# Optimization experiments

Measured on AMD Instinct MI355X. Metric: run time of the kernel, lower is better.

The kernel has to match this reference:

```python
import jax, jax.numpy as jnp
import numpy as np
from jax import lax

B, CIN, H, W = 16, 128, 56, 56
COUT, K, STRIDE, PAD, DIL = 256, 3, 1, 1, 1
D = 8  # lattice.d
KE = K * K
M = CIN * KE // D  # sub-vectors per spatial position


def setup_inputs() -> dict:
    key = jax.random.key(0)
    k1, k2, k3 = jax.random.split(key, 3)
    input_encodings = jax.random.normal(k1, (B, CIN, H, W), dtype=jnp.float32)
    weight_encodings = jax.random.normal(k2, (COUT, M, D), dtype=jnp.float32)
    bias = jax.random.normal(k3, (COUT,), dtype=jnp.float32)
    return {"input_encodings": input_encodings,
            "weight_encodings": weight_encodings,
            "bias": bias}


def reference(input_encodings, weight_encodings, bias):
    b, cin, h, w = input_encodings.shape
    cout, m, d = weight_encodings.shape
    h_out = (h + 2 * PAD - DIL * (K - 1) - 1) // STRIDE + 1
    w_out = (w + 2 * PAD - DIL * (K - 1) - 1) // STRIDE + 1
    L = h_out * w_out
    # im2col / unfold: (B, Cin*K*K, Hout, Wout), channel-major (c, kh, kw) ordering
    patches = lax.conv_general_dilated_patches(
        input_encodings, (K, K), (STRIDE, STRIDE), [(PAD, PAD), (PAD, PAD)],
        rhs_dilation=(DIL, DIL))
    # (B, L, M, D): each position split into M lattice-encoded sub-vectors of dim D
    x = patches.reshape(b, cin * K * K, L).transpose(0, 2, 1).reshape(b, L, m, d)
    # two-sided vLUT matrix multiply == sum of per-sub-vector inner products
    out = jnp.einsum('blmd,omd->bol', x, weight_encodings)  # (B, Cout, L)
    out = out.reshape(b, cout, h_out, w_out)
    return out + bias[None, :, None, None]
```

## Files before the change

kernel.cpp:

```cpp
#include <hip/hip_runtime.h>
#include <hip/hip_bf16.h>

#define CIN_   128
#define HW_    56
#define LHW_   3136
#define COUT_  256
#define KTOT_  1152

typedef unsigned short u16;
typedef __attribute__((ext_vector_type(8))) short short8v;
typedef __attribute__((ext_vector_type(4))) float f32x4;

__device__ __forceinline__ u16 f2bf(float f) {
  union { float f; unsigned u; } v; v.f = f;
  unsigned u = v.u;
  u += 0x7fffu + ((u >> 16) & 1u);
  return (u16)(u >> 16);
}
__device__ __forceinline__ unsigned pack2(u16 a, u16 b) {
  return (unsigned)a | ((unsigned)b << 16);
}

__global__ void wreorder2_kernel(const float* __restrict__ w, u16* __restrict__ wb,
                                 u16* __restrict__ zp) {
  if (blockIdx.x == 0 && threadIdx.x < 16) {
    uint4 z; z.x = z.y = z.z = z.w = 0u;
    reinterpret_cast<uint4*>(zp)[threadIdx.x] = z;
  }
  int j = blockIdx.x * 256 + threadIdx.x;
  int c4 = j & 31;
  int o  = (j >> 5) & 255;
  int t  = j >> 13;
  int c0i = c4 >> 3;
  int lg  = (c4 >> 1) & 3;
  size_t slot = ((size_t)(t * 4 + c0i) * 16 + (o >> 4)) * 64 + lg * 16 + (o & 15);
  const float* src = w + (size_t)o * KTOT_ + t;
  ushort4 r;
  r.x = f2bf(src[(c4 * 4 + 0) * 9]);
  r.y = f2bf(src[(c4 * 4 + 1) * 9]);
  r.z = f2bf(src[(c4 * 4 + 2) * 9]);
  r.w = f2bf(src[(c4 * 4 + 3) * 9]);
  *reinterpret_cast<ushort4*>(wb + slot * 8 + (c4 & 1) * 4) = r;
}

__global__ void wreorder_kernel(const float* __restrict__ w, u16* __restrict__ wb) {
  int j = blockIdx.x * 256 + threadIdx.x;
  int c4 = j & 31;
  int o  = (j >> 5) & 255;
  int t  = j >> 13;
  const float* src = w + (size_t)o * KTOT_ + t;
  ushort4 r;
  r.x = f2bf(src[(c4 * 4 + 0) * 9]);
  r.y = f2bf(src[(c4 * 4 + 1) * 9]);
  r.z = f2bf(src[(c4 * 4 + 2) * 9]);
  r.w = f2bf(src[(c4 * 4 + 3) * 9]);
  *reinterpret_cast<ushort4*>(wb + ((size_t)(t * 256 + o) * 128 + c4 * 4)) = r;
}

#define TLDSW_ 136
__global__ __launch_bounds__(256) void nhwc_kernel(
    const float* __restrict__ in, u16* __restrict__ xin) {
  __shared__ u16 ts[64 * TLDSW_];
  const int bp = blockIdx.x;
  const int b = bp / 49;
  const int pos0 = (bp % 49) * 64;
  const int tid = threadIdx.x;
  const float* ib = in + (size_t)b * CIN_ * LHW_ + pos0;
  {
    const int p  = tid & 63;
    const int c0 = (tid >> 6) * 32;
    #pragma unroll
    for (int i = 0; i < 32; ++i)
      ts[p * TLDSW_ + c0 + i] = f2bf(ib[(size_t)(c0 + i) * LHW_ + p]);
  }
  __syncthreads();
  {
    const int p  = tid >> 2;
    const int c0 = (tid & 3) * 32;
    u16* dst = xin + ((size_t)b * LHW_ + pos0 + p) * CIN_ + c0;
    const u16* srcr = &ts[p * TLDSW_ + c0];
    #pragma unroll
    for (int j = 0; j < 4; ++j)
      reinterpret_cast<uint4*>(dst)[j] =
          *reinterpret_cast<const uint4*>(srcr + j * 8);
  }
}

__device__ __forceinline__ void gload_lds16(const void* g, void* l) {
  __builtin_amdgcn_global_load_lds(
      (const __attribute__((address_space(1))) void*)g,
      (__attribute__((address_space(3))) void*)l, 16, 0, 0);
}

__global__ __launch_bounds__(256, 3) void conv6_kernel(
    const u16* __restrict__ xin, const u16* __restrict__ wb2,
    const float* __restrict__ bias, const u16* __restrict__ zpage,
    float* __restrict__ out)
{
  __shared__ __align__(16) u16 alds[2][4096];
  __shared__ __align__(16) u16 blds[2][4096];

  const int tid  = threadIdx.x;
  const int lane = tid & 63;
  const int wid  = tid >> 6;
  const int wc   = wid & 1;
  const int ws   = wid >> 1;
  const int lr   = lane & 15;
  const int lg   = lane >> 4;

  const int g   = (blockIdx.x & 7) * 98 + (blockIdx.x >> 3);
  const int coh = g & 1;
  const int nt  = g >> 1;

  const int p   = tid & 127;
  const int lgi = tid >> 7;
  const int n   = nt * 128 + p;
  const int bb  = n / LHW_;
  const int ll  = n - bb * LHW_;
  const int py  = ll / HW_;
  const int px  = ll - py * HW_;
  const u16* bsrc0 = xin + (size_t)n * CIN_ + lgi * 8;

  auto stage = [&](int ks, int h) {
    {
      const u16* s0 = wb2 + ((size_t)ks * 1024 + coh * 512 + tid) * 8;
      gload_lds16(s0,        &alds[h][(size_t)(tid & ~63) * 8]);
      gload_lds16(s0 + 2048, &alds[h][(size_t)((tid + 256) & ~63) * 8]);
    }
    {
      const int t   = ks >> 2;
      const int c0i = ks & 3;
      const int dy  = t / 3;
      const int dx  = t - dy * 3;
      const int yy  = py + dy - 1;
      const int xx  = px + dx - 1;
      const bool ok = ((unsigned)yy < (unsigned)HW_) & ((unsigned)xx < (unsigned)HW_);
      const u16* sB  = ok ? bsrc0 + ((dy - 1) * HW_ + (dx - 1)) * CIN_ + c0i * 32
                          : zpage;
      const u16* sB1 = ok ? sB + 16 : zpage;
      gload_lds16(sB,  &blds[h][(size_t)(tid & ~63) * 8]);
      gload_lds16(sB1, &blds[h][(size_t)((tid + 256) & ~63) * 8]);
    }
  };

  f32x4 acc[4][4];
  #pragma unroll
  for (int i = 0; i < 4; ++i)
    #pragma unroll
    for (int j = 0; j < 4; ++j)
      acc[i][j] = f32x4{0.f, 0.f, 0.f, 0.f};

  stage(0, 0);
  __syncthreads();

  #pragma unroll 1
  for (int ks = 0; ks < 36; ++ks) {
    const int h = ks & 1;
    if (ks < 35) stage(ks + 1, h ^ 1);

    short8v a[4], b[4];
    #pragma unroll
    for (int ai = 0; ai < 4; ++ai)
      a[ai] = *reinterpret_cast<const short8v*>(
          &alds[h][(size_t)((wc * 4 + ai) * 64 + lg * 16 + lr) * 8]);
    #pragma unroll
    for (int nj = 0; nj < 4; ++nj)
      b[nj] = *reinterpret_cast<const short8v*>(
          &blds[h][(size_t)(lg * 128 + ws * 64 + nj * 16 + lr) * 8]);

    #pragma unroll
    for (int ai = 0; ai < 4; ++ai)
      #pragma unroll
      for (int nj = 0; nj < 4; ++nj)
        acc[ai][nj] = __builtin_amdgcn_mfma_f32_16x16x32_bf16(
            a[ai], b[nj], acc[ai][nj], 0, 0, 0);

    __syncthreads();
  }

  #pragma unroll
  for (int nj = 0; nj < 4; ++nj) {
    const int nb0 = nt * 128 + ws * 64 + nj * 16;
    const int ob  = nb0 / LHW_;
    const int ol  = nb0 - ob * LHW_;
    float* obp = out + (size_t)ob * COUT_ * LHW_ + ol + lr;
    #pragma unroll
    for (int ai = 0; ai < 4; ++ai) {
      #pragma unroll
      for (int rr = 0; rr < 4; ++rr) {
        const int o = coh * 128 + wc * 64 + ai * 16 + lg * 4 + rr;
        obp[(size_t)o * LHW_] = acc[ai][nj][rr] + bias[o];
      }
    }
  }
}

#define NF_    7
#define SCOLS_ 58
#define SPP_   232
#define CSTR_  128
__global__ __launch_bounds__(256, 2) void conv2_kernel(
    const float* __restrict__ in, const u16* __restrict__ wb,
    const float* __restrict__ bias, float* __restrict__ out)
{
  __shared__ u16 xs[SPP_ * CSTR_];
  const int tid  = threadIdx.x;
  const int lane = tid & 63;
  const int wid  = tid >> 6;
  const int lr   = lane & 15;
  const int lg   = lane >> 4;
  const int bid = blockIdx.x;
  const int ch  = bid & 1;
  const int ty  = (bid >> 1) % 28;
  const int b   = bid / 56;
  const float* inb = in + (size_t)b * CIN_ * LHW_;
  const int iy0 = ty * 2 - 1;

  #pragma unroll 1
  for (int i = 0; i < 15; ++i) {
    int idx = i * 256 + tid;
    if (idx < SPP_ * 16) {
      int cg  = idx / SPP_;
      int spp = idx - cg * SPP_;
      int rr  = spp / SCOLS_;
      int cc  = spp - rr * SCOLS_;
      int iy  = iy0 + rr;
      int ix  = cc - 1;
      bool ok = ((unsigned)iy < (unsigned)HW_) && ((unsigned)ix < (unsigned)HW_);
      const float* pp = inb + (size_t)cg * 8 * LHW_ + iy * HW_ + ix;
      u16 v[8];
      #pragma unroll
      for (int jj = 0; jj < 8; ++jj)
        v[jj] = f2bf(ok ? pp[jj * LHW_] : 0.f);
      uint4 pk;
      pk.x = pack2(v[0], v[1]); pk.y = pack2(v[2], v[3]);
      pk.z = pack2(v[4], v[5]); pk.w = pack2(v[6], v[7]);
      *reinterpret_cast<uint4*>(&xs[spp * CSTR_ + ((cg * 8) ^ ((spp & 7) << 3))]) = pk;
    }
  }
  int spp0[NF_];
  #pragma unroll
  for (int nf = 0; nf < NF_; ++nf) {
    int sp = nf * 16 + lr;
    int r  = (sp >= 56) ? 1 : 0;
    int x  = sp - r * 56;
    spp0[nf] = (r + 1) * SCOLS_ + x + 1;
  }
  f32x4 acc[2][NF_];
  #pragma unroll
  for (int m = 0; m < 2; ++m)
    #pragma unroll
    for (int nf = 0; nf < NF_; ++nf)
      acc[m][nf] = f32x4{0.f, 0.f, 0.f, 0.f};
  __syncthreads();
  const u16* wt0 = wb + (size_t)(ch * 128 + wid * 32 + lr) * CSTR_ + lg * 8;
  #pragma unroll 1
  for (int t = 0; t < 9; ++t) {
    const int dspp = (t / 3 - 1) * SCOLS_ + (t % 3 - 1);
    const u16* wt = wt0 + (size_t)t * 256 * CSTR_;
    #pragma unroll
    for (int c0i = 0; c0i < 4; ++c0i) {
      const int c0 = c0i * 32;
      short8v a0 = *reinterpret_cast<const short8v*>(wt + c0);
      short8v a1 = *reinterpret_cast<const short8v*>(wt + 16 * CSTR_ + c0);
      short8v bv[NF_];
      #pragma unroll
      for (int nf = 0; nf < NF_; ++nf) {
        int spp = spp0[nf] + dspp;
        int off = spp * CSTR_ + ((c0 + lg * 8) ^ ((spp & 7) << 3));
        bv[nf] = *reinterpret_cast<const short8v*>(&xs[off]);
      }
      #pragma unroll
      for (int nf = 0; nf < NF_; ++nf) {
        acc[0][nf] = __builtin_amdgcn_mfma_f32_16x16x32_bf16(a0, bv[nf], acc[0][nf], 0, 0, 0);
        acc[1][nf] = __builtin_amdgcn_mfma_f32_16x16x32_bf16(a1, bv[nf], acc[1][nf], 0, 0, 0);
      }
    }
  }
  float* ob = out + (size_t)b * COUT_ * LHW_ + ty * 112;
  const int obase = ch * 128 + wid * 32 + lg * 4;
  #pragma unroll
  for (int m = 0; m < 2; ++m)
    #pragma unroll
    for (int rr = 0; rr < 4; ++rr) {
      const int o = obase + m * 16 + rr;
      const float bs = bias[o];
      #pragma unroll
      for (int nf = 0; nf < NF_; ++nf)
        ob[(size_t)o * LHW_ + nf * 16 + lr] = acc[m][nf][rr] + bs;
    }
}

#define SPT0_  64
#define BK0_   32
#define NKS0_  36
#define LDSW0_ 40
__global__ __launch_bounds__(256, 2) void conv_fb_kernel(
    const float* __restrict__ in, const float* __restrict__ wf,
    const float* __restrict__ bias, float* __restrict__ out)
{
  __shared__ u16 xs[SPT0_ * LDSW0_];
  const int tid = threadIdx.x;
  const int lane = tid & 63;
  const int wid = tid >> 6;
  const int lg = lane >> 4;
  const int lr = lane & 15;
  const int bid = blockIdx.x;
  const int b = bid / 49;
  const int l0 = (bid % 49) * SPT0_;
  const int sp = tid & 63;
  const int qq = tid >> 6;
  const int l = l0 + sp;
  const int y = l / HW_;
  const int x = l - y * HW_;
  const float* inb = in + (size_t)b * CIN_ * LHW_;
  f32x4 acc[4][4];
  #pragma unroll
  for (int i = 0; i < 4; ++i)
    #pragma unroll
    for (int j = 0; j < 4; ++j) acc[i][j] = f32x4{0.f, 0.f, 0.f, 0.f};
  auto stage_load = [&](int ks) -> uint4 {
    int kbase = ks * BK0_ + qq * 8;
    int c = kbase / 9;
    int t = kbase - c * 9;
    u16 v[8];
    #pragma unroll
    for (int j = 0; j < 8; ++j) {
      int dy = (t * 11) >> 5;
      int dx = t - 3 * dy;
      int yy = y + dy - 1, xx = x + dx - 1;
      float f = 0.f;
      if ((unsigned)yy < (unsigned)HW_ && (unsigned)xx < (unsigned)HW_)
        f = inb[(c * HW_ + yy) * HW_ + xx];
      v[j] = f2bf(f);
      ++t; if (t == 9) { t = 0; ++c; }
    }
    uint4 r;
    r.x = pack2(v[0], v[1]); r.y = pack2(v[2], v[3]);
    r.z = pack2(v[4], v[5]); r.w = pack2(v[6], v[7]);
    return r;
  };
  uint4 st = stage_load(0);
  for (int ks = 0; ks < NKS0_; ++ks) {
    __syncthreads();
    *reinterpret_cast<uint4*>(&xs[sp * LDSW0_ + qq * 8]) = st;
    __syncthreads();
    if (ks + 1 < NKS0_) st = stage_load(ks + 1);
    const int k0 = ks * BK0_;
    short8v a[4];
    #pragma unroll
    for (int ai = 0; ai < 4; ++ai) {
      const int o = wid * 64 + ai * 16 + lr;
      const float* pp = wf + (size_t)o * KTOT_ + k0 + lg * 8;
      u16 t8[8];
      #pragma unroll
      for (int j = 0; j < 8; ++j) t8[j] = f2bf(pp[j]);
      union { uint4 u; short8v s; } cv;
      cv.u.x = pack2(t8[0], t8[1]); cv.u.y = pack2(t8[2], t8[3]);
      cv.u.z = pack2(t8[4], t8[5]); cv.u.w = pack2(t8[6], t8[7]);
      a[ai] = cv.s;
    }
    short8v bv[4];
    #pragma unroll
    for (int sj = 0; sj < 4; ++sj)
      bv[sj] = *reinterpret_cast<const short8v*>(&xs[(sj * 16 + lr) * LDSW0_ + lg * 8]);
    #pragma unroll
    for (int ai = 0; ai < 4; ++ai)
      #pragma unroll
      for (int sj = 0; sj < 4; ++sj)
        acc[ai][sj] = __builtin_amdgcn_mfma_f32_16x16x32_bf16(a[ai], bv[sj], acc[ai][sj], 0, 0, 0);
  }
  float* outb = out + (size_t)b * COUT_ * LHW_ + l0;
  #pragma unroll
  for (int ai = 0; ai < 4; ++ai)
    #pragma unroll
    for (int r = 0; r < 4; ++r) {
      const int o = wid * 64 + ai * 16 + lg * 4 + r;
      const float bvs = bias[o];
      #pragma unroll
      for (int sj = 0; sj < 4; ++sj)
        outb[(size_t)o * LHW_ + sj * 16 + lr] = acc[ai][sj][r] + bvs;
    }
}

extern "C" void kernel_launch(void* const* d_in, const int* in_sizes, int n_in,
                              void* d_out, int out_size, void* d_ws, size_t ws_size,
                              hipStream_t stream) {
  (void)in_sizes; (void)n_in; (void)out_size;
  const float* in   = (const float*)d_in[0];
  const float* w    = (const float*)d_in[1];
  const float* bias = (const float*)d_in[2];
  float* out = (float*)d_out;

  const size_t wbytes  = (size_t)COUT_ * KTOT_ * sizeof(u16);
  const size_t xbytes  = (size_t)16 * LHW_ * CIN_ * sizeof(u16);
  const size_t need    = wbytes + xbytes + 256;

  if (ws_size >= need) {
    u16* wb2 = (u16*)d_ws;
    u16* xin = wb2 + wbytes / 2;
    u16* zp  = xin + xbytes / 2;
    wreorder2_kernel<<<dim3(288), dim3(256), 0, stream>>>(w, wb2, zp);
    nhwc_kernel<<<dim3(784), dim3(256), 0, stream>>>(in, xin);
    conv6_kernel<<<dim3(784), dim3(256), 0, stream>>>(xin, wb2, bias, zp, out);
  } else if (ws_size >= wbytes) {
    u16* wb = (u16*)d_ws;
    wreorder_kernel<<<dim3(288), dim3(256), 0, stream>>>(w, wb);
    conv2_kernel<<<dim3(896), dim3(256), 0, stream>>>(in, wb, bias, out);
  } else {
    conv_fb_kernel<<<dim3(784), dim3(256), 0, stream>>>(in, w, bias, out);
  }
}
```

Baseline: 70.03 us.

## Enlarge conv tile to 256x256 with 8-wave blocks and phased MFMA schedule

Replaces the 128x128-tile implicit-GEMM conv kernel with a 512-thread, 256(cout)x256(positions) tile that covers all output channels per block and uses a K-step of 64. Weights are re-laid out to match, and each k-step is split into four MFMA phases separated by barriers, with ds_reads interleaved and s_setprio raised around the MFMAs. The aim is more data reuse per LDS load, fewer k-iterations and better MFMA/memory overlap. In exchange it uses a 128 KB LDS double buffer and 32 accumulator tiles per wave, and launches only 196 blocks, which is below one block per CU on a 256-CU part.

After: 79.31 us. 1.13x slower.

```diff
diff --git a/kernel.cpp b/kernel.cpp
--- a/kernel.cpp
+++ b/kernel.cpp
@@ -21,26 +21,26 @@
   return (unsigned)a | ((unsigned)b << 16);
 }
 
-__global__ void wreorder2_kernel(const float* __restrict__ w, u16* __restrict__ wb,
+__global__ void wreorder3_kernel(const float* __restrict__ w, u16* __restrict__ wb3,
                                  u16* __restrict__ zp) {
   if (blockIdx.x == 0 && threadIdx.x < 16) {
     uint4 z; z.x = z.y = z.z = z.w = 0u;
     reinterpret_cast<uint4*>(zp)[threadIdx.x] = z;
   }
   int j = blockIdx.x * 256 + threadIdx.x;
-  int c4 = j & 31;
-  int o  = (j >> 5) & 255;
-  int t  = j >> 13;
-  int c0i = c4 >> 3;
-  int lg  = (c4 >> 1) & 3;
-  size_t slot = ((size_t)(t * 4 + c0i) * 16 + (o >> 4)) * 64 + lg * 16 + (o & 15);
-  const float* src = w + (size_t)o * KTOT_ + t;
+  int half = j & 1;
+  int s    = j >> 1;
+  int o    = s & 255;
+  int kg8  = s >> 8;
+  int kt   = kg8 >> 3;
+  int kgrp = kg8 & 7;
+  int t    = kt >> 1;
+  int c    = ((kt & 1) << 6) + kgrp * 8 + half * 4;
+  const float* src = w + (size_t)o * KTOT_ + (size_t)c * 9 + t;
   ushort4 r;
-  r.x = f2bf(src[(c4 * 4 + 0) * 9]);
-  r.y = f2bf(src[(c4 * 4 + 1) * 9]);
-  r.z = f2bf(src[(c4 * 4 + 2) * 9]);
-  r.w = f2bf(src[(c4 * 4 + 3) * 9]);
-  *reinterpret_cast<ushort4*>(wb + slot * 8 + (c4 & 1) * 4) = r;
+  r.x = f2bf(src[0]);  r.y = f2bf(src[9]);
+  r.z = f2bf(src[18]); r.w = f2bf(src[27]);
+  *reinterpret_cast<ushort4*>(wb3 + (size_t)s * 8 + half * 4) = r;
 }
 
 __global__ void wreorder_kernel(const float* __restrict__ w, u16* __restrict__ wb) {
@@ -92,107 +92,140 @@
       (__attribute__((address_space(3))) void*)l, 16, 0, 0);
 }
 
-__global__ __launch_bounds__(256, 3) void conv6_kernel(
-    const u16* __restrict__ xin, const u16* __restrict__ wb2,
+__global__ __launch_bounds__(512, 2) void conv7_kernel(
+    const u16* __restrict__ xin, const u16* __restrict__ wb3,
     const float* __restrict__ bias, const u16* __restrict__ zpage,
     float* __restrict__ out)
 {
-  __shared__ __align__(16) u16 alds[2][4096];
-  __shared__ __align__(16) u16 blds[2][4096];
+  __shared__ __align__(16) u16 alds[2][16384];
+  __shared__ __align__(16) u16 blds[2][16384];
 
   const int tid  = threadIdx.x;
   const int lane = tid & 63;
   const int wid  = tid >> 6;
-  const int wc   = wid & 1;
-  const int ws   = wid >> 1;
+  const int wm   = wid & 1;
+  const int wn   = wid >> 1;
   const int lr   = lane & 15;
   const int lg   = lane >> 4;
 
-  const int g   = (blockIdx.x & 7) * 98 + (blockIdx.x >> 3);
-  const int coh = g & 1;
-  const int nt  = g >> 1;
-
-  const int p   = tid & 127;
-  const int lgi = tid >> 7;
-  const int n   = nt * 128 + p;
-  const int bb  = n / LHW_;
-  const int ll  = n - bb * LHW_;
+  const int nt = blockIdx.x;
+
+  const int sp  = tid & 255;
+  const int kg0 = tid >> 8;
+  const int n   = nt * 256 + sp;
+  const int ll  = n % LHW_;
   const int py  = ll / HW_;
   const int px  = ll - py * HW_;
-  const u16* bsrc0 = xin + (size_t)n * CIN_ + lgi * 8;
-
-  auto stage = [&](int ks, int h) {
-    {
-      const u16* s0 = wb2 + ((size_t)ks * 1024 + coh * 512 + tid) * 8;
-      gload_lds16(s0,        &alds[h][(size_t)(tid & ~63) * 8]);
-      gload_lds16(s0 + 2048, &alds[h][(size_t)((tid + 256) & ~63) * 8]);
-    }
-    {
-      const int t   = ks >> 2;
-      const int c0i = ks & 3;
-      const int dy  = t / 3;
-      const int dx  = t - dy * 3;
-      const int yy  = py + dy - 1;
-      const int xx  = px + dx - 1;
-      const bool ok = ((unsigned)yy < (unsigned)HW_) & ((unsigned)xx < (unsigned)HW_);
-      const u16* sB  = ok ? bsrc0 + ((dy - 1) * HW_ + (dx - 1)) * CIN_ + c0i * 32
-                          : zpage;
-      const u16* sB1 = ok ? sB + 16 : zpage;
-      gload_lds16(sB,  &blds[h][(size_t)(tid & ~63) * 8]);
-      gload_lds16(sB1, &blds[h][(size_t)((tid + 256) & ~63) * 8]);
-    }
+  const u16* xpos = xin + (size_t)n * CIN_ + (kg0 << 3);
+  unsigned okm = 0;
+  #pragma unroll
+  for (int t = 0; t < 9; ++t) {
+    int yy = py + t / 3 - 1, xx = px + t % 3 - 1;
+    if ((unsigned)yy < (unsigned)HW_ && (unsigned)xx < (unsigned)HW_)
+      okm |= 1u << t;
+  }
+
+  const int ldsoff = (tid & ~63) * 8;
+
+  auto stage = [&](int kt, int h) {
+    const u16* sa = wb3 + ((size_t)kt * 2048 + tid) * 8;
+    u16* da = alds[h] + ldsoff;
+    #pragma unroll
+    for (int q = 0; q < 4; ++q)
+      gload_lds16(sa + q * 4096, da + q * 4096);
+    const int t    = kt >> 1;
+    const int dy   = t / 3, dx = t - dy * 3;
+    const int doff = ((dy - 1) * HW_ + (dx - 1)) * CIN_ + ((kt & 1) << 6);
+    const bool ok  = (okm >> t) & 1;
+    const u16* sb  = ok ? xpos + doff : zpage;
+    u16* db = blds[h] + ldsoff;
+    #pragma unroll
+    for (int q = 0; q < 4; ++q)
+      gload_lds16(sb + q * 16, db + q * 4096);
   };
 
-  f32x4 acc[4][4];
-  #pragma unroll
-  for (int i = 0; i < 4; ++i)
+  const int abase = (lg * 256 + wm * 128 + lr) * 8;
+  const int bbase = (lg * 256 + wn * 64 + lr) * 8;
+
+  f32x4 acc[8][4];
+  #pragma unroll
+  for (int i = 0; i < 8; ++i)
     #pragma unroll
     for (int j = 0; j < 4; ++j)
       acc[i][j] = f32x4{0.f, 0.f, 0.f, 0.f};
 
+  short8v Af[8];
+  short8v Bf0[4], Bf1[4];
+
+#define READ_A(h, half)                                                         \
+  { _Pragma("unroll") for (int kk = 0; kk < 2; ++kk)                            \
+    _Pragma("unroll") for (int ai = 0; ai < 4; ++ai)                            \
+      Af[kk * 4 + ai] = *reinterpret_cast<const short8v*>(                      \
+          &alds[h][abase + kk * 8192 + ((half) * 4 + ai) * 128]); }
+#define READ_B(h, half, Bf)                                                     \
+  { _Pragma("unroll") for (int kk = 0; kk < 2; ++kk)                            \
+    _Pragma("unroll") for (int nj = 0; nj < 2; ++nj)                            \
+      (Bf)[kk * 2 + nj] = *reinterpret_cast<const short8v*>(                    \
+          &blds[h][bbase + kk * 8192 + ((half) * 2 + nj) * 128]); }
+#define PHASE_SYNC()                                                            \
+  __builtin_amdgcn_sched_barrier(0);                                            \
+  __builtin_amdgcn_s_barrier();                                                 \
+  asm volatile("s_waitcnt lgkmcnt(0)" ::: "memory");                            \
+  __builtin_amdgcn_sched_barrier(0);
+#define MFMA16(ah, bh, Bf)                                                      \
+  { __builtin_amdgcn_s_setprio(1);                                              \
+    _Pragma("unroll") for (int kk = 0; kk < 2; ++kk)                            \
+    _Pragma("unroll") for (int ai = 0; ai < 4; ++ai)                            \
+    _Pragma("unroll") for (int nj = 0; nj < 2; ++nj)                            \
+      acc[(ah) * 4 + ai][(bh) * 2 + nj] = __builtin_amdgcn_mfma_f32_16x16x32_bf16( \
+          Af[kk * 4 + ai], (Bf)[kk * 2 + nj], acc[(ah) * 4 + ai][(bh) * 2 + nj], \
+          0, 0, 0);                                                             \
+    __builtin_amdgcn_s_setprio(0);                                              \
+    __builtin_amdgcn_sched_barrier(0);                                          \
+    __builtin_amdgcn_s_barrier(); }
+
   stage(0, 0);
-  __syncthreads();
+  asm volatile("s_waitcnt vmcnt(0)" ::: "memory");
+  __builtin_amdgcn_s_barrier();
 
   #pragma unroll 1
-  for (int ks = 0; ks < 36; ++ks) {
-    const int h = ks & 1;
-    if (ks < 35) stage(ks + 1, h ^ 1);
-
-    short8v a[4], b[4];
-    #pragma unroll
-    for (int ai = 0; ai < 4; ++ai)
-      a[ai] = *reinterpret_cast<const short8v*>(
-          &alds[h][(size_t)((wc * 4 + ai) * 64 + lg * 16 + lr) * 8]);
-    #pragma unroll
-    for (int nj = 0; nj < 4; ++nj)
-      b[nj] = *reinterpret_cast<const short8v*>(
-          &blds[h][(size_t)(lg * 128 + ws * 64 + nj * 16 + lr) * 8]);
-
-    #pragma unroll
-    for (int ai = 0; ai < 4; ++ai)
-      #pragma unroll
-      for (int nj = 0; nj < 4; ++nj)
-        acc[ai][nj] = __builtin_amdgcn_mfma_f32_16x16x32_bf16(
-            a[ai], b[nj], acc[ai][nj], 0, 0, 0);
-
-    __syncthreads();
+  for (int kt = 0; kt < 18; ++kt) {
+    const int h = kt & 1;
+    if (kt < 17) stage(kt + 1, h ^ 1);
+    READ_A(h, 0); READ_B(h, 0, Bf0);
+    PHASE_SYNC();
+    MFMA16(0, 0, Bf0);
+    READ_B(h, 1, Bf1);
+    PHASE_SYNC();
+    MFMA16(0, 1, Bf1);
+    READ_A(h, 1);
+    PHASE_SYNC();
+    MFMA16(1, 0, Bf0);
+    MFMA16(1, 1, Bf1);
+    asm volatile("s_waitcnt vmcnt(0)" ::: "memory");
+    __builtin_amdgcn_s_barrier();
   }
 
   #pragma unroll
   for (int nj = 0; nj < 4; ++nj) {
-    const int nb0 = nt * 128 + ws * 64 + nj * 16;
+    const int nb0 = nt * 256 + wn * 64 + nj * 16;
     const int ob  = nb0 / LHW_;
     const int ol  = nb0 - ob * LHW_;
     float* obp = out + (size_t)ob * COUT_ * LHW_ + ol + lr;
     #pragma unroll
-    for (int ai = 0; ai < 4; ++ai) {
-      #pragma unroll
-      for (int rr = 0; rr < 4; ++rr) {
-        const int o = coh * 128 + wc * 64 + ai * 16 + lg * 4 + rr;
-        obp[(size_t)o * LHW_] = acc[ai][nj][rr] + bias[o];
-      }
-    }
-  }
+    for (int ai = 0; ai < 8; ++ai) {
+      const int o = wm * 128 + ai * 16 + lg * 4;
+      const float4 bs = *reinterpret_cast<const float4*>(&bias[o]);
+      obp[(size_t)(o + 0) * LHW_] = acc[ai][nj][0] + bs.x;
+      obp[(size_t)(o + 1) * LHW_] = acc[ai][nj][1] + bs.y;
+      obp[(size_t)(o + 2) * LHW_] = acc[ai][nj][2] + bs.z;
+      obp[(size_t)(o + 3) * LHW_] = acc[ai][nj][3] + bs.w;
+    }
+  }
+#undef READ_A
+#undef READ_B
+#undef PHASE_SYNC
+#undef MFMA16
 }
 
 #define NF_    7
@@ -397,12 +430,12 @@
   const size_t need    = wbytes + xbytes + 256;
 
   if (ws_size >= need) {
-    u16* wb2 = (u16*)d_ws;
-    u16* xin = wb2 + wbytes / 2;
+    u16* wb3 = (u16*)d_ws;
+    u16* xin = wb3 + wbytes / 2;
     u16* zp  = xin + xbytes / 2;
-    wreorder2_kernel<<<dim3(288), dim3(256), 0, stream>>>(w, wb2, zp);
+    wreorder3_kernel<<<dim3(288), dim3(256), 0, stream>>>(w, wb3, zp);
     nhwc_kernel<<<dim3(784), dim3(256), 0, stream>>>(in, xin);
-    conv6_kernel<<<dim3(784), dim3(256), 0, stream>>>(xin, wb2, bias, zp, out);
+    conv7_kernel<<<dim3(196), dim3(512), 0, stream>>>(xin, wb3, bias, zp, out);
   } else if (ws_size >= wbytes) {
     u16* wb = (u16*)d_ws;
     wreorder_kernel<<<dim3(288), dim3(256), 0, stream>>>(w, wb);
```

## Restructure conv weight layout, merge barriers, precompute halo mask in implicit GEMM

Applied to the files above, without the earlier changes.

Reorders the packed bf16 weights into a new layout so the A and B LDS tiles share the same per-thread staging offset and fragment addressing. The main loop now waits on vmcnt and hits one barrier per k-step before issuing the next stage, instead of two __syncthreads. The 3x3 boundary-validity mask is precomputed once per thread, and bias is loaded as float4. Occupancy is raised to 4 blocks per SM. Having only one barrier depends on correct double-buffer ordering, and the higher launch bound may squeeze registers.

Measured after the change: 69.98 us. Within noise of the previous version (-0.1%).

```diff
diff --git a/kernel.cpp b/kernel.cpp
--- a/kernel.cpp
+++ b/kernel.cpp
@@ -21,26 +21,25 @@
   return (unsigned)a | ((unsigned)b << 16);
 }
 
-__global__ void wreorder2_kernel(const float* __restrict__ w, u16* __restrict__ wb,
+__global__ void wreorder5_kernel(const float* __restrict__ w, u16* __restrict__ wb5,
                                  u16* __restrict__ zp) {
   if (blockIdx.x == 0 && threadIdx.x < 16) {
     uint4 z; z.x = z.y = z.z = z.w = 0u;
     reinterpret_cast<uint4*>(zp)[threadIdx.x] = z;
   }
   int j = blockIdx.x * 256 + threadIdx.x;
-  int c4 = j & 31;
-  int o  = (j >> 5) & 255;
-  int t  = j >> 13;
-  int c0i = c4 >> 3;
-  int lg  = (c4 >> 1) & 3;
-  size_t slot = ((size_t)(t * 4 + c0i) * 16 + (o >> 4)) * 64 + lg * 16 + (o & 15);
-  const float* src = w + (size_t)o * KTOT_ + t;
+  int half = j & 1;
+  int s    = j >> 1;
+  int o    = s & 255;
+  int kgrp = (s >> 8) & 3;
+  int kt   = s >> 10;
+  int t    = kt >> 2;
+  int ch   = (kt & 3) * 32 + kgrp * 8 + half * 4;
+  const float* src = w + (size_t)o * KTOT_ + (size_t)ch * 9 + t;
   ushort4 r;
-  r.x = f2bf(src[(c4 * 4 + 0) * 9]);
-  r.y = f2bf(src[(c4 * 4 + 1) * 9]);
-  r.z = f2bf(src[(c4 * 4 + 2) * 9]);
-  r.w = f2bf(src[(c4 * 4 + 3) * 9]);
-  *reinterpret_cast<ushort4*>(wb + slot * 8 + (c4 & 1) * 4) = r;
+  r.x = f2bf(src[0]);  r.y = f2bf(src[9]);
+  r.z = f2bf(src[18]); r.w = f2bf(src[27]);
+  *reinterpret_cast<ushort4*>(wb5 + (size_t)s * 8 + half * 4) = r;
 }
 
 __global__ void wreorder_kernel(const float* __restrict__ w, u16* __restrict__ wb) {
@@ -92,8 +91,8 @@
       (__attribute__((address_space(3))) void*)l, 16, 0, 0);
 }
 
-__global__ __launch_bounds__(256, 3) void conv6_kernel(
-    const u16* __restrict__ xin, const u16* __restrict__ wb2,
+__global__ __launch_bounds__(256, 4) void conv12_kernel(
+    const u16* __restrict__ xin, const u16* __restrict__ wb5,
     const float* __restrict__ bias, const u16* __restrict__ zpage,
     float* __restrict__ out)
 {
@@ -103,8 +102,8 @@
   const int tid  = threadIdx.x;
   const int lane = tid & 63;
   const int wid  = tid >> 6;
-  const int wc   = wid & 1;
-  const int ws   = wid >> 1;
+  const int wm   = wid & 1;
+  const int wn   = wid >> 1;
   const int lr   = lane & 15;
   const int lg   = lane >> 4;
 
@@ -113,35 +112,38 @@
   const int nt  = g >> 1;
 
   const int p   = tid & 127;
-  const int lgi = tid >> 7;
+  const int kga = tid >> 7;
   const int n   = nt * 128 + p;
-  const int bb  = n / LHW_;
-  const int ll  = n - bb * LHW_;
+  const int ll  = n % LHW_;
   const int py  = ll / HW_;
   const int px  = ll - py * HW_;
-  const u16* bsrc0 = xin + (size_t)n * CIN_ + lgi * 8;
-
-  auto stage = [&](int ks, int h) {
-    {
-      const u16* s0 = wb2 + ((size_t)ks * 1024 + coh * 512 + tid) * 8;
-      gload_lds16(s0,        &alds[h][(size_t)(tid & ~63) * 8]);
-      gload_lds16(s0 + 2048, &alds[h][(size_t)((tid + 256) & ~63) * 8]);
-    }
-    {
-      const int t   = ks >> 2;
-      const int c0i = ks & 3;
-      const int dy  = t / 3;
-      const int dx  = t - dy * 3;
-      const int yy  = py + dy - 1;
-      const int xx  = px + dx - 1;
-      const bool ok = ((unsigned)yy < (unsigned)HW_) & ((unsigned)xx < (unsigned)HW_);
-      const u16* sB  = ok ? bsrc0 + ((dy - 1) * HW_ + (dx - 1)) * CIN_ + c0i * 32
-                          : zpage;
-      const u16* sB1 = ok ? sB + 16 : zpage;
-      gload_lds16(sB,  &blds[h][(size_t)(tid & ~63) * 8]);
-      gload_lds16(sB1, &blds[h][(size_t)((tid + 256) & ~63) * 8]);
-    }
+  const u16* xp = xin + (size_t)n * CIN_ + kga * 8;
+  unsigned okm = 0;
+  #pragma unroll
+  for (int t = 0; t < 9; ++t) {
+    int yy = py + t / 3 - 1, xx = px + t % 3 - 1;
+    if ((unsigned)yy < (unsigned)HW_ && (unsigned)xx < (unsigned)HW_)
+      okm |= 1u << t;
+  }
+
+  const int ldso = (tid & ~63) * 8;
+
+  auto stage = [&](int kt, int h) {
+    const u16* sa = wb5 + ((size_t)kt * 1024 + kga * 256 + coh * 128 + p) * 8;
+    gload_lds16(sa,        alds[h] + ldso);
+    gload_lds16(sa + 4096, alds[h] + ldso + 2048);
+    const int t    = kt >> 2;
+    const int dy   = t / 3, dx = t - dy * 3;
+    const int doff = ((dy - 1) * HW_ + (dx - 1)) * CIN_ + ((kt & 3) << 5);
+    const bool ok  = (okm >> t) & 1;
+    const u16* sb  = ok ? xp + doff : zpage;
+    const u16* sb1 = ok ? sb + 16 : zpage;
+    gload_lds16(sb,  blds[h] + ldso);
+    gload_lds16(sb1, blds[h] + ldso + 2048);
   };
+
+  const int abase = (lg * 128 + wm * 64 + lr) * 8;
+  const int bbase = (lg * 128 + wn * 64 + lr) * 8;
 
   f32x4 acc[4][4];
   #pragma unroll
@@ -151,46 +153,45 @@
       acc[i][j] = f32x4{0.f, 0.f, 0.f, 0.f};
 
   stage(0, 0);
-  __syncthreads();
 
   #pragma unroll 1
-  for (int ks = 0; ks < 36; ++ks) {
-    const int h = ks & 1;
-    if (ks < 35) stage(ks + 1, h ^ 1);
-
-    short8v a[4], b[4];
+  for (int kt = 0; kt < 36; ++kt) {
+    const int h = kt & 1;
+    asm volatile("s_waitcnt vmcnt(0)" ::: "memory");
+    __builtin_amdgcn_s_barrier();
+    asm volatile("" ::: "memory");
+    if (kt < 35) stage(kt + 1, h ^ 1);
+
+    short8v a[4], bv[4];
     #pragma unroll
     for (int ai = 0; ai < 4; ++ai)
-      a[ai] = *reinterpret_cast<const short8v*>(
-          &alds[h][(size_t)((wc * 4 + ai) * 64 + lg * 16 + lr) * 8]);
+      a[ai] = *reinterpret_cast<const short8v*>(&alds[h][abase + ai * 128]);
     #pragma unroll
     for (int nj = 0; nj < 4; ++nj)
-      b[nj] = *reinterpret_cast<const short8v*>(
-          &blds[h][(size_t)(lg * 128 + ws * 64 + nj * 16 + lr) * 8]);
-
+      bv[nj] = *reinterpret_cast<const short8v*>(&blds[h][bbase + nj * 128]);
     #pragma unroll
     for (int ai = 0; ai < 4; ++ai)
       #pragma unroll
       for (int nj = 0; nj < 4; ++nj)
         acc[ai][nj] = __builtin_amdgcn_mfma_f32_16x16x32_bf16(
-            a[ai], b[nj], acc[ai][nj], 0, 0, 0);
-
-    __syncthreads();
+            a[ai], bv[nj], acc[ai][nj], 0, 0, 0);
+    asm volatile("" ::: "memory");
   }
 
   #pragma unroll
   for (int nj = 0; nj < 4; ++nj) {
-    const int nb0 = nt * 128 + ws * 64 + nj * 16;
+    const int nb0 = nt * 128 + wn * 64 + nj * 16;
     const int ob  = nb0 / LHW_;
     const int ol  = nb0 - ob * LHW_;
     float* obp = out + (size_t)ob * COUT_ * LHW_ + ol + lr;
     #pragma unroll
     for (int ai = 0; ai < 4; ++ai) {
-      #pragma unroll
-      for (int rr = 0; rr < 4; ++rr) {
-        const int o = coh * 128 + wc * 64 + ai * 16 + lg * 4 + rr;
-        obp[(size_t)o * LHW_] = acc[ai][nj][rr] + bias[o];
-      }
+      const int o = coh * 128 + wm * 64 + ai * 16 + lg * 4;
+      const float4 bs = *reinterpret_cast<const float4*>(&bias[o]);
+      obp[(size_t)(o + 0) * LHW_] = acc[ai][nj][0] + bs.x;
+      obp[(size_t)(o + 1) * LHW_] = acc[ai][nj][1] + bs.y;
+      obp[(size_t)(o + 2) * LHW_] = acc[ai][nj][2] + bs.z;
+      obp[(size_t)(o + 3) * LHW_] = acc[ai][nj][3] + bs.w;
     }
   }
 }
@@ -397,12 +398,12 @@
   const size_t need    = wbytes + xbytes + 256;
 
   if (ws_size >= need) {
-    u16* wb2 = (u16*)d_ws;
-    u16* xin = wb2 + wbytes / 2;
+    u16* wb5 = (u16*)d_ws;
+    u16* xin = wb5 + wbytes / 2;
     u16* zp  = xin + xbytes / 2;
-    wreorder2_kernel<<<dim3(288), dim3(256), 0, stream>>>(w, wb2, zp);
+    wreorder5_kernel<<<dim3(288), dim3(256), 0, stream>>>(w, wb5, zp);
     nhwc_kernel<<<dim3(784), dim3(256), 0, stream>>>(in, xin);
-    conv6_kernel<<<dim3(784), dim3(256), 0, stream>>>(xin, wb2, bias, zp, out);
+    conv12_kernel<<<dim3(784), dim3(256), 0, stream>>>(xin, wb5, bias, zp, out);
   } else if (ws_size >= wbytes) {
     u16* wb = (u16*)d_ws;
     wreorder_kernel<<<dim3(288), dim3(256), 0, stream>>>(w, wb);
```
